# Kernel tuning notes

Hardware: AMD Instinct MI355X
Metric: run time of the kernel (lower is better)

The kernel has to match this reference:

```python
import jax, jax.numpy as jnp
import numpy as np


def setup_inputs() -> dict:
    key = jax.random.key(0)
    k1, k2, k3 = jax.random.split(key, 3)
    early = jax.random.normal(k1, (64, 1, 512, 512), dtype=jnp.float32)
    middle = jax.random.normal(k2, (64, 1, 256, 256), dtype=jnp.float32)
    deep = jax.random.normal(k3, (64, 1, 128, 128), dtype=jnp.float32)
    return {"early": early, "middle": middle, "deep": deep, "max_features": 500000}


def reference(early, middle, deep, max_features):
    # Concatenate all scores and find the threshold = (max_features)-th entry of
    # the descending sort, i.e. the (max_features+1)-th largest value.
    all_scores = jnp.concatenate([early.ravel(), middle.ravel(), deep.ravel()])
    n = all_scores.shape[0]
    if max_features >= n:
        thresh = jnp.asarray(0.0, dtype=all_scores.dtype)
    else:
        # top_k(k+1)[-1] == sort(descending)[k]; avoids a full sort.
        topk_vals, _ = jax.lax.top_k(all_scores, max_features + 1)
        thresh = topk_vals[-1]
    thresh = jax.lax.stop_gradient(thresh)
    early_out = jnp.where(early < thresh, jnp.zeros((), early.dtype), early)
    middle_out = jnp.where(middle < thresh, jnp.zeros((), middle.dtype), middle)
    deep_out = jnp.where(deep < thresh, jnp.zeros((), deep.dtype), deep)
    return (early_out, middle_out, deep_out)
```

## Files before the change

### kernel.cpp

```cpp
#include <hip/hip_runtime.h>

typedef float nfloat4 __attribute__((ext_vector_type(4)));

#define WS_CANDCNT 0
#define WS_HIST1   16
#define WS_HIST2   272
#define WS_HIST3   4368
#define WS_ZEND    8464
#define WS_CAND    8464

#define STASH 1024

__device__ __forceinline__ unsigned fkey(float f) {
  unsigned x = __float_as_uint(f);
  return x ^ ((x & 0x80000000u) ? 0xFFFFFFFFu : 0x80000000u);
}
__device__ __forceinline__ float unkey(unsigned u) {
  unsigned x = u ^ ((u & 0x80000000u) ? 0x80000000u : 0xFFFFFFFFu);
  return __uint_as_float(x);
}

__device__ __forceinline__ unsigned block_scan_incl(unsigned v, unsigned* sh4) {
  const int t = threadIdx.x;
  unsigned p = v;
#pragma unroll
  for (int off = 1; off < 64; off <<= 1) {
    unsigned y = __shfl_up(p, off);
    if ((t & 63) >= off) p += y;
  }
  if ((t & 63) == 63) sh4[t >> 6] = p;
  __syncthreads();
  unsigned wo = 0;
  for (int w = 0; w < (t >> 6); ++w) wo += sh4[w];
  __syncthreads();
  return p + wo;
}

__device__ __forceinline__ uint2 select_desc256(const unsigned* __restrict__ gh,
                                                unsigned k, unsigned* sh4, unsigned* sel2) {
  const int t = threadIdx.x;
  unsigned cnt = gh[255 - t];
  unsigned incl = block_scan_incl(cnt, sh4);
  unsigned excl = incl - cnt;
  if (excl < k && incl >= k) { sel2[0] = (unsigned)(255 - t); sel2[1] = k - excl; }
  __syncthreads();
  uint2 r; r.x = sel2[0]; r.y = sel2[1];
  __syncthreads();
  return r;
}

__device__ __forceinline__ uint2 select_desc4096(const unsigned* __restrict__ gh,
                                                 unsigned k, unsigned* sh4, unsigned* sel2) {
  const int t = threadIdx.x;
  unsigned loc[16]; unsigned s = 0;
  const int base = 4095 - t * 16;
#pragma unroll
  for (int j = 0; j < 16; ++j) { unsigned c = gh[base - j]; loc[j] = c; s += c; }
  unsigned incl = block_scan_incl(s, sh4);
  unsigned excl = incl - s;
  if (excl < k && incl >= k) {
    unsigned cum = excl; int j = 0;
    while (cum + loc[j] < k) { cum += loc[j]; ++j; }
    sel2[0] = (unsigned)(base - j); sel2[1] = k - cum;
  }
  __syncthreads();
  uint2 r; r.x = sel2[0]; r.y = sel2[1];
  __syncthreads();
  return r;
}

__global__ void zero_ws(unsigned* __restrict__ ws) {
  int i = blockIdx.x * blockDim.x + threadIdx.x;
  if (i < WS_ZEND) ws[i] = 0u;
}

__global__ void __launch_bounds__(512) hist1_kernel(
    const float* __restrict__ e, const float* __restrict__ m,
    const float* __restrict__ d, int n0v, int n1v, int n2v,
    unsigned* __restrict__ ws) {
  __shared__ unsigned h[256 * 32];
  for (int i = threadIdx.x; i < 256 * 32; i += 512) h[i] = 0u;
  __syncthreads();
  const unsigned sub = threadIdx.x & 31u;
  const int gid = blockIdx.x * 512 + threadIdx.x;
  const int G = gridDim.x * 512;

  auto acc1 = [&](float4 f) {
    atomicAdd(&h[((fkey(f.x) >> 24) << 5) | sub], 1u);
    atomicAdd(&h[((fkey(f.y) >> 24) << 5) | sub], 1u);
    atomicAdd(&h[((fkey(f.z) >> 24) << 5) | sub], 1u);
    atomicAdd(&h[((fkey(f.w) >> 24) << 5) | sub], 1u);
  };
  auto sweep = [&](const float* src, int nv) {
    const float4* a4 = (const float4*)src;
    int v = gid;
    for (; v + 3 * G < nv; v += 4 * G) {
      float4 f0 = a4[v];
      float4 f1 = a4[v + G];
      float4 f2 = a4[v + 2 * G];
      float4 f3 = a4[v + 3 * G];
      acc1(f0); acc1(f1); acc1(f2); acc1(f3);
    }
    for (; v < nv; v += G) acc1(a4[v]);
  };
  sweep(e, n0v);
  sweep(m, n1v);
  sweep(d, n2v);
  __syncthreads();
  const int t = threadIdx.x;
  if (t < 256) {
    unsigned s = 0;
#pragma unroll
    for (int j = 0; j < 32; ++j) s += h[(t << 5) + ((t + j) & 31)];
    if (s) atomicAdd(&ws[WS_HIST1 + t], s);
  }
}

__global__ void __launch_bounds__(256) scatter_kernel(
    const float* __restrict__ e, const float* __restrict__ m, const float* __restrict__ d,
    float* __restrict__ out, const int* __restrict__ maxf,
    unsigned* __restrict__ ws, unsigned cap,
    int e_blks, int m_blks, long long n) {
  const int t = threadIdx.x;
  const int bid = blockIdx.x;

  __shared__ float    sh_v[STASH];
  __shared__ unsigned sh_i[STASH];
  __shared__ unsigned sh_cnt;
  __shared__ unsigned sh_base;
  __shared__ unsigned sh4[4];
  __shared__ unsigned sel2[2];

  if (t == 0) sh_cnt = 0u;

  long long kk = (long long)maxf[0] + 1;
  unsigned b1;
  if (kk > n) {
    b1 = 0x80u;
    __syncthreads();
  } else {
    uint2 r = select_desc256(ws + WS_HIST1, (unsigned)kk, sh4, sel2);
    b1 = r.x;
  }

  const float4* in4;
  if (bid < e_blks)               in4 = (const float4*)e + (long long)bid * 2048;
  else if (bid < e_blks + m_blks) in4 = (const float4*)m + (long long)(bid - e_blks) * 2048;
  else                            in4 = (const float4*)d + (long long)(bid - e_blks - m_blks) * 2048;
  const int out_base_v = bid * 2048;
  nfloat4* out4 = (nfloat4*)out + out_base_v;

  float* gcV = (float*)(ws + WS_CAND);
  unsigned* gcI = ws + WS_CAND + cap;

  auto emit1 = [&](float4 f, int v) {
    unsigned kx = fkey(f.x), ky = fkey(f.y), kz = fkey(f.z), kw = fkey(f.w);
    nfloat4 o;
    o.x = ((kx >> 24) >= b1) ? f.x : 0.0f;
    o.y = ((ky >> 24) >= b1) ? f.y : 0.0f;
    o.z = ((kz >> 24) >= b1) ? f.z : 0.0f;
    o.w = ((kw >> 24) >= b1) ? f.w : 0.0f;
    __builtin_nontemporal_store(o, &out4[v]);
    unsigned ks[4] = {kx, ky, kz, kw};
    float fs[4] = {f.x, f.y, f.z, f.w};
#pragma unroll
    for (int cc = 0; cc < 4; ++cc) {
      if ((ks[cc] >> 24) == b1) {
        unsigned idx = (unsigned)(out_base_v + v) * 4u + (unsigned)cc;
        unsigned pos = atomicAdd(&sh_cnt, 1u);
        if (pos < STASH) { sh_v[pos] = fs[cc]; sh_i[pos] = idx; }
        else {
          unsigned g = atomicAdd(&ws[WS_CANDCNT], 1u);
          gcV[g] = fs[cc]; gcI[g] = idx;
        }
      }
    }
  };

#pragma unroll
  for (int g = 0; g < 2; ++g) {
    const int v0 = (g * 4 + 0) * 256 + t;
    const int v1 = (g * 4 + 1) * 256 + t;
    const int v2 = (g * 4 + 2) * 256 + t;
    const int v3 = (g * 4 + 3) * 256 + t;
    float4 f0 = in4[v0];
    float4 f1 = in4[v1];
    float4 f2 = in4[v2];
    float4 f3 = in4[v3];
    emit1(f0, v0); emit1(f1, v1); emit1(f2, v2); emit1(f3, v3);
  }

  __syncthreads();
  if (t == 0) {
    unsigned tot = sh_cnt < STASH ? sh_cnt : STASH;
    sh_base = tot ? atomicAdd(&ws[WS_CANDCNT], tot) : 0u;
    sh_cnt = tot;
  }
  __syncthreads();
  const unsigned tot = sh_cnt;
  const unsigned base = sh_base;
  for (unsigned i = t; i < tot; i += 256) {
    gcV[base + i] = sh_v[i];
    gcI[base + i] = sh_i[i];
  }
}

__global__ void __launch_bounds__(256) candhist2_kernel(
    unsigned* __restrict__ ws, unsigned cap) {
  const int t = threadIdx.x;
  __shared__ unsigned sh_hist[4096];
  for (int i = t; i < 4096; i += 256) sh_hist[i] = 0u;
  __syncthreads();
  unsigned cnt = ws[WS_CANDCNT]; if (cnt > cap) cnt = cap;
  const float* candV = (const float*)(ws + WS_CAND);
  const unsigned G = gridDim.x * 256;
  for (unsigned i = blockIdx.x * 256 + t; i < cnt; i += G) {
    unsigned u = fkey(candV[i]);
    atomicAdd(&sh_hist[(u >> 12) & 0xFFFu], 1u);
  }
  __syncthreads();
  for (int i = t; i < 4096; i += 256) {
    unsigned v = sh_hist[i];
    if (v) atomicAdd(&ws[WS_HIST2 + i], v);
  }
}

__global__ void __launch_bounds__(256) candhist3_kernel(
    const int* __restrict__ maxf, unsigned* __restrict__ ws, unsigned cap, long long n) {
  const int t = threadIdx.x;
  __shared__ unsigned sh_hist[4096];
  __shared__ unsigned sh4[4];
  __shared__ unsigned sel2[2];
  for (int i = t; i < 4096; i += 256) sh_hist[i] = 0u;

  long long kk = (long long)maxf[0] + 1;
  unsigned pfx;
  if (kk > n) {
    pfx = 0x80u << 12;
    __syncthreads();
  } else {
    uint2 r1 = select_desc256(ws + WS_HIST1, (unsigned)kk, sh4, sel2);
    uint2 r2 = select_desc4096(ws + WS_HIST2, r1.y, sh4, sel2);
    pfx = (r1.x << 12) | r2.x;
  }
  __syncthreads();

  unsigned cnt = ws[WS_CANDCNT]; if (cnt > cap) cnt = cap;
  const float* candV = (const float*)(ws + WS_CAND);
  const unsigned G = gridDim.x * 256;
  for (unsigned i = blockIdx.x * 256 + t; i < cnt; i += G) {
    unsigned u = fkey(candV[i]);
    if ((u >> 12) == pfx) atomicAdd(&sh_hist[u & 0xFFFu], 1u);
  }
  __syncthreads();
  for (int i = t; i < 4096; i += 256) {
    unsigned v = sh_hist[i];
    if (v) atomicAdd(&ws[WS_HIST3 + i], v);
  }
}

__global__ void __launch_bounds__(256) fixup_kernel(
    float* __restrict__ out, const int* __restrict__ maxf,
    unsigned* __restrict__ ws, unsigned cap, long long n) {
  const int t = threadIdx.x;
  __shared__ unsigned sh4[4];
  __shared__ unsigned sel2[2];

  long long kk = (long long)maxf[0] + 1;
  float th;
  if (kk > n) {
    th = 0.0f;
    __syncthreads();
  } else {
    uint2 r1 = select_desc256(ws + WS_HIST1, (unsigned)kk, sh4, sel2);
    uint2 r2 = select_desc4096(ws + WS_HIST2, r1.y, sh4, sel2);
    uint2 r3 = select_desc4096(ws + WS_HIST3, r2.y, sh4, sel2);
    th = unkey((r1.x << 24) | (r2.x << 12) | r3.x);
  }

  unsigned cnt = ws[WS_CANDCNT]; if (cnt > cap) cnt = cap;
  const float* candV = (const float*)(ws + WS_CAND);
  const unsigned* candI = ws + WS_CAND + cap;
  const unsigned G = gridDim.x * 256;
  for (unsigned i = blockIdx.x * 256 + t; i < cnt; i += G) {
    float f = candV[i];
    if (f < th) out[candI[i]] = 0.0f;
  }
}

extern "C" void kernel_launch(void* const* d_in, const int* in_sizes, int n_in,
                              void* d_out, int out_size, void* d_ws, size_t ws_size,
                              hipStream_t stream) {
  const float* e = (const float*)d_in[0];
  const float* m = (const float*)d_in[1];
  const float* d = (const float*)d_in[2];
  const int* maxf = (const int*)d_in[3];
  float* out = (float*)d_out;
  unsigned* ws = (unsigned*)d_ws;

  const long long n0 = in_sizes[0], n1 = in_sizes[1], n2 = in_sizes[2];
  const long long n = n0 + n1 + n2;
  const int n0v = (int)(n0 / 4), n1v = (int)(n1 / 4), n2v = (int)(n2 / 4);

  long long capll = ((long long)(ws_size / 4) - WS_CAND) / 2;
  if (capll < 0) capll = 0;
  if (capll > n) capll = n;
  const unsigned cap = (unsigned)capll;

  const int e_blks = (int)(n0 / 8192), m_blks = (int)(n1 / 8192);
  const int nblocks = (int)(n / 8192);

  zero_ws<<<(WS_ZEND + 255) / 256, 256, 0, stream>>>(ws);
  hist1_kernel<<<1024, 512, 0, stream>>>(e, m, d, n0v, n1v, n2v, ws);
  scatter_kernel<<<nblocks, 256, 0, stream>>>(e, m, d, out, maxf, ws, cap, e_blks, m_blks, n);
  candhist2_kernel<<<128, 256, 0, stream>>>(ws, cap);
  candhist3_kernel<<<128, 256, 0, stream>>>(maxf, ws, cap, n);
  fixup_kernel<<<256, 256, 0, stream>>>(out, maxf, ws, cap, n);
}
```

Before: 251.6 us.

## Hoist first-pass bucket selection into a single-block kernel, widen scatter blocks

The coarse bucket selection over the 256-bin histogram was redone by every scatter block. It now runs once in a dedicated one-block kernel, which writes the chosen bucket to the workspace for the scatter kernel to read. The scatter kernel moves to 1024 threads, each handling two float4 loads instead of eight, and the shared stash is doubled. The histogram kernel also moves to 512 blocks of 1024 threads. This removes redundant per-block scan and sync work at the cost of an extra kernel launch and less per-thread memory-level parallelism.

New measurement: 211.4 us. -16.0%, faster.

```diff
diff --git a/kernel.cpp b/kernel.cpp
--- a/kernel.cpp
+++ b/kernel.cpp
@@ -3,13 +3,14 @@
 typedef float nfloat4 __attribute__((ext_vector_type(4)));
 
 #define WS_CANDCNT 0
+#define WS_B1      1
 #define WS_HIST1   16
 #define WS_HIST2   272
 #define WS_HIST3   4368
 #define WS_ZEND    8464
 #define WS_CAND    8464
 
-#define STASH 1024
+#define STASH 2048
 
 __device__ __forceinline__ unsigned fkey(float f) {
   unsigned x = __float_as_uint(f);
@@ -74,16 +75,16 @@
   if (i < WS_ZEND) ws[i] = 0u;
 }
 
-__global__ void __launch_bounds__(512) hist1_kernel(
+__global__ void __launch_bounds__(1024) hist1_kernel(
     const float* __restrict__ e, const float* __restrict__ m,
     const float* __restrict__ d, int n0v, int n1v, int n2v,
     unsigned* __restrict__ ws) {
   __shared__ unsigned h[256 * 32];
-  for (int i = threadIdx.x; i < 256 * 32; i += 512) h[i] = 0u;
+  for (int i = threadIdx.x; i < 256 * 32; i += 1024) h[i] = 0u;
   __syncthreads();
   const unsigned sub = threadIdx.x & 31u;
-  const int gid = blockIdx.x * 512 + threadIdx.x;
-  const int G = gridDim.x * 512;
+  const int gid = blockIdx.x * 1024 + threadIdx.x;
+  const int G = gridDim.x * 1024;
 
   auto acc1 = [&](float4 f) {
     atomicAdd(&h[((fkey(f.x) >> 24) << 5) | sub], 1u);
@@ -116,11 +117,23 @@
   }
 }
 
-__global__ void __launch_bounds__(256) scatter_kernel(
+__global__ void __launch_bounds__(256) sel1_kernel(
+    const int* __restrict__ maxf, unsigned* __restrict__ ws, long long n) {
+  __shared__ unsigned sh4[4];
+  __shared__ unsigned sel2[2];
+  long long kk = (long long)maxf[0] + 1;
+  if (kk > n) {
+    if (threadIdx.x == 0) ws[WS_B1] = 0x80u;
+    return;
+  }
+  uint2 r = select_desc256(ws + WS_HIST1, (unsigned)kk, sh4, sel2);
+  if (threadIdx.x == 0) ws[WS_B1] = r.x;
+}
+
+__global__ void __launch_bounds__(1024) scatter_kernel(
     const float* __restrict__ e, const float* __restrict__ m, const float* __restrict__ d,
-    float* __restrict__ out, const int* __restrict__ maxf,
-    unsigned* __restrict__ ws, unsigned cap,
-    int e_blks, int m_blks, long long n) {
+    float* __restrict__ out, unsigned* __restrict__ ws, unsigned cap,
+    int e_blks, int m_blks) {
   const int t = threadIdx.x;
   const int bid = blockIdx.x;
 
@@ -128,20 +141,10 @@
   __shared__ unsigned sh_i[STASH];
   __shared__ unsigned sh_cnt;
   __shared__ unsigned sh_base;
-  __shared__ unsigned sh4[4];
-  __shared__ unsigned sel2[2];
 
   if (t == 0) sh_cnt = 0u;
-
-  long long kk = (long long)maxf[0] + 1;
-  unsigned b1;
-  if (kk > n) {
-    b1 = 0x80u;
-    __syncthreads();
-  } else {
-    uint2 r = select_desc256(ws + WS_HIST1, (unsigned)kk, sh4, sel2);
-    b1 = r.x;
-  }
+  const unsigned b1 = ws[WS_B1];
+  __syncthreads();
 
   const float4* in4;
   if (bid < e_blks)               in4 = (const float4*)e + (long long)bid * 2048;
@@ -177,18 +180,12 @@
     }
   };
 
-#pragma unroll
-  for (int g = 0; g < 2; ++g) {
-    const int v0 = (g * 4 + 0) * 256 + t;
-    const int v1 = (g * 4 + 1) * 256 + t;
-    const int v2 = (g * 4 + 2) * 256 + t;
-    const int v3 = (g * 4 + 3) * 256 + t;
-    float4 f0 = in4[v0];
-    float4 f1 = in4[v1];
-    float4 f2 = in4[v2];
-    float4 f3 = in4[v3];
-    emit1(f0, v0); emit1(f1, v1); emit1(f2, v2); emit1(f3, v3);
-  }
+  const int v0 = t;
+  const int v1 = 1024 + t;
+  float4 f0 = in4[v0];
+  float4 f1 = in4[v1];
+  emit1(f0, v0);
+  emit1(f1, v1);
 
   __syncthreads();
   if (t == 0) {
@@ -199,7 +196,7 @@
   __syncthreads();
   const unsigned tot = sh_cnt;
   const unsigned base = sh_base;
-  for (unsigned i = t; i < tot; i += 256) {
+  for (unsigned i = t; i < tot; i += 1024) {
     gcV[base + i] = sh_v[i];
     gcI[base + i] = sh_i[i];
   }
@@ -311,8 +308,9 @@
   const int nblocks = (int)(n / 8192);
 
   zero_ws<<<(WS_ZEND + 255) / 256, 256, 0, stream>>>(ws);
-  hist1_kernel<<<1024, 512, 0, stream>>>(e, m, d, n0v, n1v, n2v, ws);
-  scatter_kernel<<<nblocks, 256, 0, stream>>>(e, m, d, out, maxf, ws, cap, e_blks, m_blks, n);
+  hist1_kernel<<<512, 1024, 0, stream>>>(e, m, d, n0v, n1v, n2v, ws);
+  sel1_kernel<<<1, 256, 0, stream>>>(maxf, ws, n);
+  scatter_kernel<<<nblocks, 1024, 0, stream>>>(e, m, d, out, ws, cap, e_blks, m_blks);
   candhist2_kernel<<<128, 256, 0, stream>>>(ws, cap);
   candhist3_kernel<<<128, 256, 0, stream>>>(maxf, ws, cap, n);
   fixup_kernel<<<256, 256, 0, stream>>>(out, maxf, ws, cap, n);
```
